# Optimization experiments

Measured on AMD Instinct MI355X. Metric: run time of the kernel, lower is better.

The kernel has to match this reference:

```python
import jax, jax.numpy as jnp
import numpy as np

PHM_DIM = 4
IN_FEATS = 2048
OUT_FEATS = 8192
TOKENS = 8192


def setup_inputs() -> dict:
    key = jax.random.key(0)
    k_x, k_rule, k_w = jax.random.split(key, 3)
    x = jax.random.normal(k_x, (TOKENS, IN_FEATS), dtype=jnp.float32)
    # c_init='normal', std=0.01
    phm_rule = 0.01 * jax.random.normal(k_rule, (PHM_DIM, PHM_DIM, PHM_DIM), dtype=jnp.float32)
    # w_init='normal', std=phm_init_range=1e-4 (scaled up here for numerics of the test)
    W = 1e-4 * jax.random.normal(k_w, (PHM_DIM, IN_FEATS // PHM_DIM, OUT_FEATS // PHM_DIM), dtype=jnp.float32)
    b = jnp.zeros((OUT_FEATS,), dtype=jnp.float32)
    return {"x": x, "phm_rule": phm_rule, "W": W, "b": b}


def reference(x, phm_rule, W, b):
    # H = sum_i kron(phm_rule[i], W[i])  with shape (phm_dim*in_per, phm_dim*out_per)
    # kron(A, B)[a*in_per + c, k*out_per + p] = A[a, k] * B[c, p]
    d, in_per, out_per = W.shape
    H = jnp.einsum('iak,icp->acKp'.replace('K', 'k'), phm_rule, W)  # (d, in_per, d, out_per)
    H = H.reshape(d * in_per, d * out_per)
    y = x @ H + b
    return y
```

## Files before the change

### kernel.cpp

```cpp
#include <hip/hip_runtime.h>
#include <stdint.h>

#define PHM      4
#define IN_FEATS 2048
#define OUT_FEATS 8192
#define TOKENS   8192
#define IN_PER   512
#define OUT_PER  2048

typedef __attribute__((ext_vector_type(8)))  short short8;
typedef __attribute__((ext_vector_type(16))) float f32x16;
typedef __attribute__((ext_vector_type(8)))  unsigned short u16x8;

__device__ inline unsigned short f2bf(float f) {
    unsigned int u = __builtin_bit_cast(unsigned int, f);
    u += 0x7fffu + ((u >> 16) & 1u);
    return (unsigned short)(u >> 16);
}

__global__ void cvt_x_kernel(const float* __restrict__ x,
                             unsigned short* __restrict__ xb) {
    int i = blockIdx.x * blockDim.x + threadIdx.x;
    const float4* x4 = (const float4*)x;
    float4 v0 = x4[2 * i];
    float4 v1 = x4[2 * i + 1];
    u16x8 o;
    o[0] = f2bf(v0.x); o[1] = f2bf(v0.y); o[2] = f2bf(v0.z); o[3] = f2bf(v0.w);
    o[4] = f2bf(v1.x); o[5] = f2bf(v1.y); o[6] = f2bf(v1.z); o[7] = f2bf(v1.w);
    *(u16x8*)(xb + 8 * (size_t)i) = o;
}

__global__ void build_ht_kernel(const float* __restrict__ rule,
                                const float* __restrict__ W,
                                unsigned short* __restrict__ Ht)
{
    __shared__ float lds[PHM][32][65];
    const int tid = threadIdx.x;
    const int c0 = blockIdx.x * 32;
    const int p0 = blockIdx.y * 64;

    #pragma unroll
    for (int it = 0; it < 32; ++it) {
        int idx = it * 256 + tid;
        int pp = idx & 63;
        int cc = (idx >> 6) & 31;
        int i  = idx >> 11;
        lds[i][cc][pp] = W[((size_t)(i * IN_PER + c0 + cc)) * OUT_PER + p0 + pp];
    }
    __syncthreads();

    const int pp = tid >> 2;
    const int j0 = (tid & 3) * 8;
    float w[PHM][8];
    #pragma unroll
    for (int i = 0; i < PHM; ++i)
        #pragma unroll
        for (int j = 0; j < 8; ++j)
            w[i][j] = lds[i][j0 + j][pp];

    #pragma unroll
    for (int a = 0; a < PHM; ++a) {
        #pragma unroll
        for (int kq = 0; kq < PHM; ++kq) {
            float r0 = rule[(0 * PHM + a) * PHM + kq];
            float r1 = rule[(1 * PHM + a) * PHM + kq];
            float r2 = rule[(2 * PHM + a) * PHM + kq];
            float r3 = rule[(3 * PHM + a) * PHM + kq];
            u16x8 o;
            #pragma unroll
            for (int j = 0; j < 8; ++j) {
                float v = r0 * w[0][j] + r1 * w[1][j] + r2 * w[2][j] + r3 * w[3][j];
                o[j] = f2bf(v);
            }
            size_t n = (size_t)(kq * OUT_PER + p0 + pp);
            *(u16x8*)(Ht + n * IN_FEATS + a * IN_PER + c0 + j0) = o;
        }
    }
}

#define BM 128
#define BN 256
#define BK 32

__device__ inline void load_lds16(const unsigned short* g, unsigned short* l) {
    __builtin_amdgcn_global_load_lds(
        (const __attribute__((address_space(1))) unsigned int*)g,
        (__attribute__((address_space(3))) unsigned int*)l,
        16, 0, 0);
}

__global__ __launch_bounds__(256, 2) void gemm_bt_kernel(
    const unsigned short* __restrict__ A,
    const unsigned short* __restrict__ B,
    const float* __restrict__ bias,
    float* __restrict__ C)
{
    constexpr int N = OUT_FEATS, K = IN_FEATS;
    __shared__ unsigned short As[BM * BK];
    __shared__ unsigned short Bs[BN * BK];

    const int tid  = threadIdx.x;
    const int wave = tid >> 6;
    const int lane = tid & 63;
    const int bn = blockIdx.x;
    const int bm = blockIdx.y;

    const int wm = (wave >> 1) * 64;
    const int wn = (wave & 1) * 128;

    const int s_row = lane >> 2;
    const int s_col = (lane & 3) * 8;

    const unsigned short* Ag = A + ((size_t)(bm * BM + wave * 32 + s_row)) * K + s_col;
    const unsigned short* Bg = B + ((size_t)(bn * BN + wave * 64 + s_row)) * K + s_col;
    unsigned short* As_w = &As[(wave * 32) * BK];
    unsigned short* Bs_w = &Bs[(wave * 64) * BK];

    const int m   = lane & 31;
    const int cg  = lane >> 5;
    const int p0o = cg * 8;
    const int p1o = (2 + cg) * 8;

    f32x16 acc[2][4] = {};

    for (int k0 = 0; k0 < K; k0 += BK) {
        __syncthreads();
        load_lds16(Ag + k0,          As_w);
        load_lds16(Ag + 16 * K + k0, As_w + 16 * BK);
        load_lds16(Bg + k0,          Bs_w);
        load_lds16(Bg + 16 * K + k0, Bs_w + 16 * BK);
        load_lds16(Bg + 32 * K + k0, Bs_w + 32 * BK);
        load_lds16(Bg + 48 * K + k0, Bs_w + 48 * BK);
        __builtin_amdgcn_s_waitcnt(0);
        __syncthreads();

        short8 a0[2], a1[2], b0[4], b1[4];
        #pragma unroll
        for (int i = 0; i < 2; ++i) {
            a0[i] = *(const short8*)&As[(wm + i * 32 + m) * BK + p0o];
            a1[i] = *(const short8*)&As[(wm + i * 32 + m) * BK + p1o];
        }
        #pragma unroll
        for (int j = 0; j < 4; ++j) {
            b0[j] = *(const short8*)&Bs[(wn + j * 32 + m) * BK + p0o];
            b1[j] = *(const short8*)&Bs[(wn + j * 32 + m) * BK + p1o];
        }
        #pragma unroll
        for (int i = 0; i < 2; ++i)
            #pragma unroll
            for (int j = 0; j < 4; ++j) {
                acc[i][j] = __builtin_amdgcn_mfma_f32_32x32x16_bf16(
                    a0[i], b0[j], acc[i][j], 0, 0, 0);
                acc[i][j] = __builtin_amdgcn_mfma_f32_32x32x16_bf16(
                    a1[i], b1[j], acc[i][j], 0, 0, 0);
            }
    }

    const int cn    = lane & 31;
    const int rbase = 4 * (lane >> 5);
    #pragma unroll
    for (int j = 0; j < 4; ++j) {
        int col = bn * BN + wn + j * 32 + cn;
        float bv = bias[col];
        #pragma unroll
        for (int i = 0; i < 2; ++i) {
            int row0 = bm * BM + wm + i * 32 + rbase;
            #pragma unroll
            for (int reg = 0; reg < 16; ++reg) {
                int row = row0 + (reg & 3) + 8 * (reg >> 2);
                C[(size_t)row * N + col] = acc[i][j][reg] + bv;
            }
        }
    }
}

extern "C" void kernel_launch(void* const* d_in, const int* in_sizes, int n_in,
                              void* d_out, int out_size, void* d_ws, size_t ws_size,
                              hipStream_t stream) {
    const float* x    = (const float*)d_in[0];
    const float* rule = (const float*)d_in[1];
    const float* W    = (const float*)d_in[2];
    const float* b    = (const float*)d_in[3];
    float* y = (float*)d_out;

    unsigned short* xb = (unsigned short*)d_ws;
    unsigned short* Ht = (unsigned short*)((char*)d_ws +
                         (size_t)TOKENS * IN_FEATS * sizeof(unsigned short));

    cvt_x_kernel<<<(TOKENS * IN_FEATS) / 8 / 256, 256, 0, stream>>>(x, xb);
    build_ht_kernel<<<dim3(IN_PER / 32, OUT_PER / 64), 256, 0, stream>>>(rule, W, Ht);
    gemm_bt_kernel<<<dim3(OUT_FEATS / BN, TOKENS / BM), 256, 0, stream>>>(xb, Ht, b, y);
}
```

Before: 609.1 us.

## Restructure bf16 GEMM with 256x256 tiles, triple-buffered LDS and XOR swizzle

The GEMM moves to 256x256 block tiles with 512 threads and triple-buffered LDS fed by global_load_lds, so the next tiles load while the current one computes. Each iteration is split into two half-phases that interleave staging and MFMA work, using barriers and setprio. LDS rows use an XOR swizzle to avoid bank conflicts, and the workgroup order is remapped for L2 locality. This targets load stalls and the serial wait-then-compute pattern, at the cost of more LDS (96KB) and registers per block and fragile manual waitcnt logic.

After: 611.6 us. About the same (+0.4%).

```diff
diff --git a/kernel.cpp b/kernel.cpp
--- a/kernel.cpp
+++ b/kernel.cpp
@@ -78,93 +78,173 @@
     }
 }
 
-#define BM 128
+#define BM 256
 #define BN 256
 #define BK 32
-
-__device__ inline void load_lds16(const unsigned short* g, unsigned short* l) {
+#define NTILES (IN_FEATS / BK)
+#define LTILE  (BM * BK)
+
+__device__ inline void gload16(const unsigned short* g, unsigned short* l) {
     __builtin_amdgcn_global_load_lds(
         (const __attribute__((address_space(1))) unsigned int*)g,
         (__attribute__((address_space(3))) unsigned int*)l,
         16, 0, 0);
 }
 
-__global__ __launch_bounds__(256, 2) void gemm_bt_kernel(
+__device__ inline void barrier_fenced() {
+    asm volatile("" ::: "memory");
+    __builtin_amdgcn_s_barrier();
+    asm volatile("" ::: "memory");
+}
+
+__global__ __launch_bounds__(512, 2) void gemm_bt_kernel(
     const unsigned short* __restrict__ A,
     const unsigned short* __restrict__ B,
     const float* __restrict__ bias,
     float* __restrict__ C)
 {
     constexpr int N = OUT_FEATS, K = IN_FEATS;
-    __shared__ unsigned short As[BM * BK];
-    __shared__ unsigned short Bs[BN * BK];
+    constexpr int NXB = OUT_FEATS / BN;
+    constexpr int NWG = (TOKENS / BM) * NXB;
+
+    __shared__ unsigned short As[3 * LTILE];
+    __shared__ unsigned short Bs[3 * LTILE];
 
     const int tid  = threadIdx.x;
     const int wave = tid >> 6;
     const int lane = tid & 63;
-    const int bn = blockIdx.x;
-    const int bm = blockIdx.y;
-
-    const int wm = (wave >> 1) * 64;
-    const int wn = (wave & 1) * 128;
-
-    const int s_row = lane >> 2;
-    const int s_col = (lane & 3) * 8;
-
-    const unsigned short* Ag = A + ((size_t)(bm * BM + wave * 32 + s_row)) * K + s_col;
-    const unsigned short* Bg = B + ((size_t)(bn * BN + wave * 64 + s_row)) * K + s_col;
-    unsigned short* As_w = &As[(wave * 32) * BK];
-    unsigned short* Bs_w = &Bs[(wave * 64) * BK];
-
-    const int m   = lane & 31;
-    const int cg  = lane >> 5;
-    const int p0o = cg * 8;
-    const int p1o = (2 + cg) * 8;
-
-    f32x16 acc[2][4] = {};
-
-    for (int k0 = 0; k0 < K; k0 += BK) {
-        __syncthreads();
-        load_lds16(Ag + k0,          As_w);
-        load_lds16(Ag + 16 * K + k0, As_w + 16 * BK);
-        load_lds16(Bg + k0,          Bs_w);
-        load_lds16(Bg + 16 * K + k0, Bs_w + 16 * BK);
-        load_lds16(Bg + 32 * K + k0, Bs_w + 32 * BK);
-        load_lds16(Bg + 48 * K + k0, Bs_w + 48 * BK);
-        __builtin_amdgcn_s_waitcnt(0);
-        __syncthreads();
-
-        short8 a0[2], a1[2], b0[4], b1[4];
-        #pragma unroll
-        for (int i = 0; i < 2; ++i) {
-            a0[i] = *(const short8*)&As[(wm + i * 32 + m) * BK + p0o];
-            a1[i] = *(const short8*)&As[(wm + i * 32 + m) * BK + p1o];
+    const int lm   = lane & 31;
+    const int kh   = lane >> 5;
+
+    const int orig = blockIdx.y * NXB + blockIdx.x;
+    const int swzb = (orig & 7) * (NWG >> 3) + (orig >> 3);
+    const int bn = swzb & (NXB - 1);
+    const int bm = swzb >> 5;
+
+    const int wm = (wave >> 2) * 128;
+    const int wn = (wave & 3) * 64;
+
+    int offA[2][2][2];
+    int offB[2][2];
+    #pragma unroll
+    for (int mh = 0; mh < 2; ++mh)
+        #pragma unroll
+        for (int mf = 0; mf < 2; ++mf)
+            #pragma unroll
+            for (int ks = 0; ks < 2; ++ks) {
+                int r   = wm + (mh * 2 + mf) * 32 + lm;
+                int k16 = ks * 2 + kh;
+                offA[mh][mf][ks] = r * BK + ((k16 ^ ((r >> 1) & 3)) << 3);
+            }
+    #pragma unroll
+    for (int nf = 0; nf < 2; ++nf)
+        #pragma unroll
+        for (int ks = 0; ks < 2; ++ks) {
+            int r   = wn + nf * 32 + lm;
+            int k16 = ks * 2 + kh;
+            offB[nf][ks] = r * BK + ((k16 ^ ((r >> 1) & 3)) << 3);
         }
-        #pragma unroll
-        for (int j = 0; j < 4; ++j) {
-            b0[j] = *(const short8*)&Bs[(wn + j * 32 + m) * BK + p0o];
-            b1[j] = *(const short8*)&Bs[(wn + j * 32 + m) * BK + p1o];
-        }
-        #pragma unroll
-        for (int i = 0; i < 2; ++i)
-            #pragma unroll
-            for (int j = 0; j < 4; ++j) {
-                acc[i][j] = __builtin_amdgcn_mfma_f32_32x32x16_bf16(
-                    a0[i], b0[j], acc[i][j], 0, 0, 0);
-                acc[i][j] = __builtin_amdgcn_mfma_f32_32x32x16_bf16(
-                    a1[i], b1[j], acc[i][j], 0, 0, 0);
-            }
-    }
-
-    const int cn    = lane & 31;
-    const int rbase = 4 * (lane >> 5);
-    #pragma unroll
-    for (int j = 0; j < 4; ++j) {
-        int col = bn * BN + wn + j * 32 + cn;
-        float bv = bias[col];
-        #pragma unroll
-        for (int i = 0; i < 2; ++i) {
-            int row0 = bm * BM + wm + i * 32 + rbase;
+
+    const int srow = tid >> 2;
+    const int scol = (((tid & 3) ^ ((tid >> 3) & 3)) << 3);
+    const unsigned short* Ag0 = A + (size_t)(bm * BM + srow) * K + scol;
+    const unsigned short* Ag1 = Ag0 + (size_t)128 * K;
+    const unsigned short* Bg0 = B + (size_t)(bn * BN + srow) * K + scol;
+    const unsigned short* Bg1 = Bg0 + (size_t)128 * K;
+    unsigned short* const As_d0 = As + wave * 16 * BK;
+    unsigned short* const As_d1 = As_d0 + 128 * BK;
+    unsigned short* const Bs_d0 = Bs + wave * 16 * BK;
+    unsigned short* const Bs_d1 = Bs_d0 + 128 * BK;
+
+    #define STAGE_A(koff, so) do { \
+        gload16(Ag0 + (koff), As_d0 + (so)); \
+        gload16(Ag1 + (koff), As_d1 + (so)); } while (0)
+    #define STAGE_B(koff, so) do { \
+        gload16(Bg0 + (koff), Bs_d0 + (so)); \
+        gload16(Bg1 + (koff), Bs_d1 + (so)); } while (0)
+
+    STAGE_A(0, 0);            STAGE_B(0, 0);
+    STAGE_A(BK, LTILE);       STAGE_B(BK, LTILE);
+    asm volatile("s_waitcnt vmcnt(4)" ::: "memory");
+    barrier_fenced();
+
+    f32x16 acc[4][2] = {};
+    int cur = 0, stg = 2;
+
+    #pragma unroll 1
+    for (int t = 0; t < NTILES; ++t) {
+        const unsigned short* Ab = As + cur * LTILE;
+        const unsigned short* Bb = Bs + cur * LTILE;
+        const bool st   = (t + 2) < NTILES;
+        const int  k2   = (t + 2) * BK;
+        const int  so   = stg * LTILE;
+
+        short8 a[2][2], b[2][2];
+
+        #pragma unroll
+        for (int mf = 0; mf < 2; ++mf)
+            #pragma unroll
+            for (int ks = 0; ks < 2; ++ks)
+                a[mf][ks] = *(const short8*)(Ab + offA[0][mf][ks]);
+        #pragma unroll
+        for (int nf = 0; nf < 2; ++nf)
+            #pragma unroll
+            for (int ks = 0; ks < 2; ++ks)
+                b[nf][ks] = *(const short8*)(Bb + offB[nf][ks]);
+        if (st) STAGE_A(k2, so);
+        barrier_fenced();
+        asm volatile("s_waitcnt lgkmcnt(0)" ::: "memory");
+        __builtin_amdgcn_sched_barrier(0);
+        __builtin_amdgcn_s_setprio(1);
+        #pragma unroll
+        for (int ks = 0; ks < 2; ++ks)
+            #pragma unroll
+            for (int mf = 0; mf < 2; ++mf)
+                #pragma unroll
+                for (int nf = 0; nf < 2; ++nf)
+                    acc[mf][nf] = __builtin_amdgcn_mfma_f32_32x32x16_bf16(
+                        a[mf][ks], b[nf][ks], acc[mf][nf], 0, 0, 0);
+        __builtin_amdgcn_s_setprio(0);
+        barrier_fenced();
+
+        #pragma unroll
+        for (int mf = 0; mf < 2; ++mf)
+            #pragma unroll
+            for (int ks = 0; ks < 2; ++ks)
+                a[mf][ks] = *(const short8*)(Ab + offA[1][mf][ks]);
+        if (st) STAGE_B(k2, so);
+        barrier_fenced();
+        asm volatile("s_waitcnt lgkmcnt(0)" ::: "memory");
+        __builtin_amdgcn_sched_barrier(0);
+        __builtin_amdgcn_s_setprio(1);
+        #pragma unroll
+        for (int ks = 0; ks < 2; ++ks)
+            #pragma unroll
+            for (int mf = 0; mf < 2; ++mf)
+                #pragma unroll
+                for (int nf = 0; nf < 2; ++nf)
+                    acc[2 + mf][nf] = __builtin_amdgcn_mfma_f32_32x32x16_bf16(
+                        a[mf][ks], b[nf][ks], acc[2 + mf][nf], 0, 0, 0);
+        __builtin_amdgcn_s_setprio(0);
+        if (t < NTILES - 2) asm volatile("s_waitcnt vmcnt(4)" ::: "memory");
+        else                asm volatile("s_waitcnt vmcnt(0)" ::: "memory");
+        barrier_fenced();
+
+        cur = (cur == 2) ? 0 : cur + 1;
+        stg = (stg == 2) ? 0 : stg + 1;
+    }
+    #undef STAGE_A
+    #undef STAGE_B
+
+    const int cn = lm;
+    const int rb = 4 * kh;
+    #pragma unroll
+    for (int j = 0; j < 2; ++j) {
+        const int col = bn * BN + wn + j * 32 + cn;
+        const float bv = bias[col];
+        #pragma unroll
+        for (int i = 0; i < 4; ++i) {
+            const int row0 = bm * BM + wm + i * 32 + rb;
             #pragma unroll
             for (int reg = 0; reg < 16; ++reg) {
                 int row = row0 + (reg & 3) + 8 * (reg >> 2);
@@ -189,5 +269,5 @@
 
     cvt_x_kernel<<<(TOKENS * IN_FEATS) / 8 / 256, 256, 0, stream>>>(x, xb);
     build_ht_kernel<<<dim3(IN_PER / 32, OUT_PER / 64), 256, 0, stream>>>(rule, W, Ht);
-    gemm_bt_kernel<<<dim3(OUT_FEATS / BN, TOKENS / BM), 256, 0, stream>>>(xb, Ht, b, y);
-}
+    gemm_bt_kernel<<<dim3(OUT_FEATS / BN, TOKENS / BM), 512, 0, stream>>>(xb, Ht, b, y);
+}
```

## Rewrite GEMM as 256x256 tile, 8-wave, double-buffered pipelined MFMA kernel

Applied to the files above, without the earlier changes.

Replaces the single-buffered 128x256 BK=32 GEMM with a 256x256 BK=64 tile run by 512 threads and 16x16x32 MFMAs. Global-to-LDS loads for the next K tile are interleaved with compute across eight phases, using vmcnt waits, barriers, setprio and an XOR-swizzled LDS layout. The aim is to hide memory latency, avoid LDS bank conflicts and raise data reuse per tile. The cost is a 128KB LDS footprint and complex hand-scheduled sync that is fragile to get right.

After: 544.8 us. -10.6%, faster.

```diff
diff --git a/kernel.cpp b/kernel.cpp
--- a/kernel.cpp
+++ b/kernel.cpp
@@ -9,7 +9,7 @@
 #define OUT_PER  2048
 
 typedef __attribute__((ext_vector_type(8)))  short short8;
-typedef __attribute__((ext_vector_type(16))) float f32x16;
+typedef __attribute__((ext_vector_type(4)))  float f32x4;
 typedef __attribute__((ext_vector_type(8)))  unsigned short u16x8;
 
 __device__ inline unsigned short f2bf(float f) {
@@ -78,100 +78,150 @@
     }
 }
 
-#define BM 128
+#define BM 256
 #define BN 256
-#define BK 32
-
-__device__ inline void load_lds16(const unsigned short* g, unsigned short* l) {
+#define BK 64
+#define NT (IN_FEATS / BK)
+
+__device__ inline void gload16(const unsigned short* g, unsigned short* l) {
     __builtin_amdgcn_global_load_lds(
         (const __attribute__((address_space(1))) unsigned int*)g,
         (__attribute__((address_space(3))) unsigned int*)l,
         16, 0, 0);
 }
 
-__global__ __launch_bounds__(256, 2) void gemm_bt_kernel(
+#define WAITV(N) asm volatile("s_waitcnt vmcnt(" #N ")" ::: "memory")
+#define LGKM0    asm volatile("s_waitcnt lgkmcnt(0)" ::: "memory")
+#define FENCE    asm volatile("" ::: "memory")
+#define SBAR     do { FENCE; __builtin_amdgcn_s_barrier(); FENCE; } while (0)
+
+__global__ __launch_bounds__(512, 2) void gemm_bt_kernel(
     const unsigned short* __restrict__ A,
     const unsigned short* __restrict__ B,
     const float* __restrict__ bias,
     float* __restrict__ C)
 {
     constexpr int N = OUT_FEATS, K = IN_FEATS;
-    __shared__ unsigned short As[BM * BK];
-    __shared__ unsigned short Bs[BN * BK];
+    __shared__ unsigned short LDS[65536];
 
     const int tid  = threadIdx.x;
     const int wave = tid >> 6;
     const int lane = tid & 63;
+    const int lm16 = lane & 15;
+    const int l47  = lane >> 4;
+
     const int bn = blockIdx.x;
     const int bm = blockIdx.y;
 
-    const int wm = (wave >> 1) * 64;
-    const int wn = (wave & 1) * 128;
-
-    const int s_row = lane >> 2;
-    const int s_col = (lane & 3) * 8;
-
-    const unsigned short* Ag = A + ((size_t)(bm * BM + wave * 32 + s_row)) * K + s_col;
-    const unsigned short* Bg = B + ((size_t)(bn * BN + wave * 64 + s_row)) * K + s_col;
-    unsigned short* As_w = &As[(wave * 32) * BK];
-    unsigned short* Bs_w = &Bs[(wave * 64) * BK];
-
-    const int m   = lane & 31;
-    const int cg  = lane >> 5;
-    const int p0o = cg * 8;
-    const int p1o = (2 + cg) * 8;
-
-    f32x16 acc[2][4] = {};
-
-    for (int k0 = 0; k0 < K; k0 += BK) {
-        __syncthreads();
-        load_lds16(Ag + k0,          As_w);
-        load_lds16(Ag + 16 * K + k0, As_w + 16 * BK);
-        load_lds16(Bg + k0,          Bs_w);
-        load_lds16(Bg + 16 * K + k0, Bs_w + 16 * BK);
-        load_lds16(Bg + 32 * K + k0, Bs_w + 32 * BK);
-        load_lds16(Bg + 48 * K + k0, Bs_w + 48 * BK);
-        __builtin_amdgcn_s_waitcnt(0);
-        __syncthreads();
-
-        short8 a0[2], a1[2], b0[4], b1[4];
+    const int wm = (wave >> 2) * 64;
+    const int wn = (wave & 3) * 32;
+
+    const int aB  = (wm + lm16) * 64;
+    const int bB  = 16384 + (wn + lm16) * 64;
+    const int sc0 = ((l47      ^ (lane & 7))) * 8;
+    const int sc1 = (((4 + l47) ^ (lane & 7))) * 8;
+
+    const int srow = tid >> 3;
+    const int schk = (lane & 7) ^ ((lane >> 3) & 7);
+    const unsigned short* AgS = A + (size_t)(bm * BM + srow) * K + schk * 8;
+    const unsigned short* BgS = B + (size_t)(bn * BN + srow) * K + schk * 8;
+
+    #define STG_A(db, h, T) do { \
+        gload16(AgS + (size_t)((h) * 128)      * K + (T) * 64, LDS + (db) + (h) * 8192        + wave * 512); \
+        gload16(AgS + (size_t)((h) * 128 + 64) * K + (T) * 64, LDS + (db) + (h) * 8192 + 4096 + wave * 512); } while (0)
+    #define STG_B(db, h, T) do { \
+        gload16(BgS + (size_t)((h) * 128)      * K + (T) * 64, LDS + 16384 + (db) + (h) * 8192        + wave * 512); \
+        gload16(BgS + (size_t)((h) * 128 + 64) * K + (T) * 64, LDS + 16384 + (db) + (h) * 8192 + 4096 + wave * 512); } while (0)
+
+    #define RD_A(D, FB) do { _Pragma("unroll") \
+        for (int ff = 0; ff < 4; ++ff) { \
+            a[ff][0] = *(const short8*)(LDS + (D) + aB + (FB) + ff * 1024 + sc0); \
+            a[ff][1] = *(const short8*)(LDS + (D) + aB + (FB) + ff * 1024 + sc1); } } while (0)
+    #define RD_B01(D) do { _Pragma("unroll") \
+        for (int g = 0; g < 2; ++g) { \
+            b[g][0] = *(const short8*)(LDS + (D) + bB + g * 1024 + sc0); \
+            b[g][1] = *(const short8*)(LDS + (D) + bB + g * 1024 + sc1); } } while (0)
+    #define RD_B23(D) do { _Pragma("unroll") \
+        for (int g = 0; g < 2; ++g) { \
+            b[2 + g][0] = *(const short8*)(LDS + (D) + bB + 8192 + g * 1024 + sc0); \
+            b[2 + g][1] = *(const short8*)(LDS + (D) + bB + 8192 + g * 1024 + sc1); } } while (0)
+
+    #define MM(FB, GB) do { _Pragma("unroll") \
+        for (int k2 = 0; k2 < 2; ++k2) { _Pragma("unroll") \
+            for (int ff = 0; ff < 4; ++ff) { _Pragma("unroll") \
+                for (int g = 0; g < 2; ++g) \
+                    acc[(FB) + ff][(GB) + g] = __builtin_amdgcn_mfma_f32_16x16x32_bf16( \
+                        a[ff][k2], b[(GB) + g][k2], acc[(FB) + ff][(GB) + g], 0, 0, 0); } } } while (0)
+
+    #define PH_MID do { SBAR; LGKM0; __builtin_amdgcn_sched_barrier(0); \
+                        __builtin_amdgcn_s_setprio(1); } while (0)
+    #define PH_END do { __builtin_amdgcn_s_setprio(0); SBAR; } while (0)
+
+    STG_A(0, 0, 0);  STG_B(0, 0, 0);  STG_B(0, 1, 0);  STG_A(0, 1, 0);
+    STG_A(32768, 0, 1);  STG_B(32768, 0, 1);  STG_B(32768, 1, 1);
+    WAITV(8);
+    SBAR;
+
+    f32x4 acc[8][4] = {};
+    short8 a[4][2], b[4][2];
+
+    #pragma unroll 1
+    for (int j = 0; j < NT / 2 - 1; ++j) {
+        const int t2 = 2 * j + 2, t3 = 2 * j + 3;
+        WAITV(8); RD_A(0, 0); RD_B01(0); STG_A(32768, 1, 2 * j + 1);
+        PH_MID; MM(0, 0); PH_END;
+        WAITV(8); RD_B23(0); STG_A(0, 0, t2);
+        PH_MID; MM(0, 2); PH_END;
+        WAITV(8); RD_A(0, 8192); STG_B(0, 0, t2);
+        PH_MID; MM(4, 0); PH_END;
+        WAITV(8); STG_B(0, 1, t2);
+        PH_MID; MM(4, 2); PH_END;
+        WAITV(8); RD_A(32768, 0); RD_B01(32768); STG_A(0, 1, t2);
+        PH_MID; MM(0, 0); PH_END;
+        WAITV(8); RD_B23(32768); STG_A(32768, 0, t3);
+        PH_MID; MM(0, 2); PH_END;
+        WAITV(8); RD_A(32768, 8192); STG_B(32768, 0, t3);
+        PH_MID; MM(4, 0); PH_END;
+        WAITV(8); STG_B(32768, 1, t3);
+        PH_MID; MM(4, 2); PH_END;
+    }
+
+    WAITV(8); RD_A(0, 0); RD_B01(0); STG_A(32768, 1, NT - 1);
+    PH_MID; MM(0, 0); PH_END;
+    WAITV(8); RD_B23(0);
+    PH_MID; MM(0, 2); PH_END;
+    WAITV(8); RD_A(0, 8192);
+    PH_MID; MM(4, 0); PH_END;
+    WAITV(4);
+    PH_MID; MM(4, 2); PH_END;
+    WAITV(2); RD_A(32768, 0); RD_B01(32768);
+    PH_MID; MM(0, 0); PH_END;
+    WAITV(0); RD_B23(32768);
+    PH_MID; MM(0, 2); PH_END;
+    RD_A(32768, 8192);
+    PH_MID; MM(4, 0); PH_END;
+    PH_MID; MM(4, 2); PH_END;
+
+    #pragma unroll
+    for (int g = 0; g < 4; ++g) {
+        const int col = bn * BN + wn + (g >> 1) * 128 + (g & 1) * 16 + lm16;
+        const float bv = bias[col];
         #pragma unroll
-        for (int i = 0; i < 2; ++i) {
-            a0[i] = *(const short8*)&As[(wm + i * 32 + m) * BK + p0o];
-            a1[i] = *(const short8*)&As[(wm + i * 32 + m) * BK + p1o];
+        for (int f = 0; f < 8; ++f) {
+            const int row0 = bm * BM + wm + (f >> 2) * 128 + (f & 3) * 16 + l47 * 4;
+            #pragma unroll
+            for (int r = 0; r < 4; ++r)
+                C[(size_t)(row0 + r) * N + col] = acc[f][g][r] + bv;
         }
-        #pragma unroll
-        for (int j = 0; j < 4; ++j) {
-            b0[j] = *(const short8*)&Bs[(wn + j * 32 + m) * BK + p0o];
-            b1[j] = *(const short8*)&Bs[(wn + j * 32 + m) * BK + p1o];
-        }
-        #pragma unroll
-        for (int i = 0; i < 2; ++i)
-            #pragma unroll
-            for (int j = 0; j < 4; ++j) {
-                acc[i][j] = __builtin_amdgcn_mfma_f32_32x32x16_bf16(
-                    a0[i], b0[j], acc[i][j], 0, 0, 0);
-                acc[i][j] = __builtin_amdgcn_mfma_f32_32x32x16_bf16(
-                    a1[i], b1[j], acc[i][j], 0, 0, 0);
-            }
-    }
-
-    const int cn    = lane & 31;
-    const int rbase = 4 * (lane >> 5);
-    #pragma unroll
-    for (int j = 0; j < 4; ++j) {
-        int col = bn * BN + wn + j * 32 + cn;
-        float bv = bias[col];
-        #pragma unroll
-        for (int i = 0; i < 2; ++i) {
-            int row0 = bm * BM + wm + i * 32 + rbase;
-            #pragma unroll
-            for (int reg = 0; reg < 16; ++reg) {
-                int row = row0 + (reg & 3) + 8 * (reg >> 2);
-                C[(size_t)row * N + col] = acc[i][j][reg] + bv;
-            }
-        }
-    }
+    }
+    #undef STG_A
+    #undef STG_B
+    #undef RD_A
+    #undef RD_B01
+    #undef RD_B23
+    #undef MM
+    #undef PH_MID
+    #undef PH_END
 }
 
 extern "C" void kernel_launch(void* const* d_in, const int* in_sizes, int n_in,
@@ -189,5 +239,5 @@
 
     cvt_x_kernel<<<(TOKENS * IN_FEATS) / 8 / 256, 256, 0, stream>>>(x, xb);
     build_ht_kernel<<<dim3(IN_PER / 32, OUT_PER / 64), 256, 0, stream>>>(rule, W, Ht);
-    gemm_bt_kernel<<<dim3(OUT_FEATS / BN, TOKENS / BM), 256, 0, stream>>>(xb, Ht, b, y);
-}
+    gemm_bt_kernel<<<dim3(OUT_FEATS / BN, TOKENS / BM), 512, 0, stream>>>(xb, Ht, b, y);
+}
```
